# Optimization experiments

Measured on AMD Instinct MI355X. Metric: run time of the kernel, lower is better.

The kernel has to match this reference:

```python
import jax, jax.numpy as jnp
import numpy as np

N, C, H, W = 4, 256, 60, 60
CIMG = 5  # rgb/ir channels after add_position (3 + x + y)
K = 8
ITERS = 2


def setup_inputs() -> dict:
    key = jax.random.key(0)
    ks = jax.random.split(key, 12)
    inp = {
        "cnn_encoder_output": jax.random.normal(ks[0], (N, C, H, W), jnp.float32),
        "rgb": jax.random.normal(ks[1], (N, CIMG, H, W), jnp.float32),
        "ir": jax.random.normal(ks[2], (N, CIMG, H, W), jnp.float32),
        # g-MLP (mlp_num_layers=1): Linear(2C -> C), torch weight layout [out, in]
        "W_g_rgb": jax.random.normal(ks[3], (C, 2 * C), jnp.float32) * 0.02,
        "b_g_rgb": jnp.zeros((C,), jnp.float32),
        "W_g_ir": jax.random.normal(ks[4], (C, 2 * C), jnp.float32) * 0.02,
        "b_g_ir": jnp.zeros((C,), jnp.float32),
        # SE block: Linear(2C -> C//16) -> ReLU -> Linear(C//16 -> C) -> Sigmoid
        "W_se1": jax.random.normal(ks[5], (C // 16, 2 * C), jnp.float32) * 0.02,
        "b_se1": jnp.zeros((C // 16,), jnp.float32),
        "W_se2": jax.random.normal(ks[6], (C, C // 16), jnp.float32) * 0.02,
        "b_se2": jnp.zeros((C,), jnp.float32),
        "gamma": jnp.ones((1,), jnp.float32),
        "gnn_iterations": ITERS,
        "k": K,
    }
    return inp


def _knn_indices(x, k):
    # x: [N, HW, D] -> indices of k nearest neighbours [N, HW, k]
    r = jnp.einsum("nid,njd->nij", x, x)          # gram matrix
    sq = jnp.einsum("nid,nid->ni", x, x)          # squared norms
    d2 = sq[:, :, None] + sq[:, None, :] - 2.0 * r
    d = jnp.sqrt(jnp.maximum(d2, 0.0))
    d = jax.lax.stop_gradient(d)
    _, idx = jax.lax.top_k(-d, k)                  # smallest distances
    return idx


def _gather(h, idx):
    # h: [N, HW, C], idx: [N, HW, K] -> [N, HW, K, C]
    return jax.vmap(lambda hn, i: hn[i])(h, idx)


def reference(cnn_encoder_output, rgb, ir, W_g_rgb, b_g_rgb, W_g_ir, b_g_ir,
              W_se1, b_se1, W_se2, b_se2, gamma, gnn_iterations, k):
    n, c, hh, ww = cnn_encoder_output.shape
    hw = hh * ww
    rgb_f = rgb.reshape(n, rgb.shape[1], hw).transpose(0, 2, 1)  # [N, HW, 5]
    ir_f = ir.reshape(n, ir.shape[1], hw).transpose(0, 2, 1)
    knn_rgb = _knn_indices(rgb_f, k)  # [N, HW, K]
    knn_ir = _knn_indices(ir_f, k)

    h = cnn_encoder_output.transpose(0, 2, 3, 1).reshape(n, hw, c)  # [N, HW, C]

    for _ in range(gnn_iterations):
        rgb_nb = _gather(h, knn_rgb)  # [N, HW, K, C]
        ir_nb = _gather(h, knn_ir)
        rgb_feat = jnp.concatenate([rgb_nb, rgb_nb - ir_nb], axis=-1)  # [N,HW,K,2C]
        ir_feat = jnp.concatenate([ir_nb, ir_nb - rgb_nb], axis=-1)
        m_rgb = jnp.max(jax.nn.relu(jnp.einsum("nhkf,cf->nhkc", rgb_feat, W_g_rgb) + b_g_rgb), axis=2)
        m_ir = jnp.max(jax.nn.relu(jnp.einsum("nhkf,cf->nhkc", ir_feat, W_g_ir) + b_g_ir), axis=2)
        cc = jnp.concatenate([m_rgb, m_ir], axis=-1).mean(axis=1, keepdims=True)  # [N,1,2C]
        se = jax.nn.sigmoid(jax.nn.relu(cc @ W_se1.T + b_se1) @ W_se2.T + b_se2)  # [N,1,C]
        h = se * h

    h = h.reshape(n, hh, ww, c).transpose(0, 3, 1, 2)
    return jax.nn.relu(gamma * h + cnn_encoder_output)
```

## Files before the change

### kernel.cpp

```cpp
#include <hip/hip_runtime.h>
#include <hip/hip_bf16.h>

#define NB 4
#define CH 256
#define HWT 3600
#define KNN 8
#define POSB 16
#define MPAD 3712

#define SSEGP 16
#define CAND 225
#define RB 8

#define GEMM_BLKS 928

typedef __attribute__((ext_vector_type(8))) __bf16 bf16x8;
typedef __attribute__((ext_vector_type(4))) float f32x4;
typedef __attribute__((ext_vector_type(4))) unsigned u32x4;

__device__ inline float med3f(float a, float b, float c) {
    return __builtin_amdgcn_fmed3f(a, b, c);
}

__device__ __forceinline__ void insert8(float* best, float kf) {
    best[7] = med3f(best[6], best[7], kf);
    best[6] = med3f(best[5], best[6], kf);
    best[5] = med3f(best[4], best[5], kf);
    best[4] = med3f(best[3], best[4], kf);
    best[3] = med3f(best[2], best[3], kf);
    best[2] = med3f(best[1], best[2], kf);
    best[1] = med3f(best[0], best[1], kf);
    best[0] = fminf(best[0], kf);
}


__device__ __forceinline__ void gemm_body(int lid, int n,
                                          const __hip_bfloat16* __restrict__ Abf,
                                          const __hip_bfloat16* __restrict__ Wbf,
                                          __hip_bfloat16* __restrict__ Yall,
                                          char* smem) {
    char* sA = smem;
    char* sB = smem + 16384;
    int w = (lid & 7) * 29 + (lid >> 3);
    int m0 = (w >> 3) * 128;
    int o0 = (w & 7) * 128;
    int t = threadIdx.x;
    int lane = t & 63, wid = t >> 6;
    int wm = wid >> 1, wo = wid & 1;

    const __hip_bfloat16* Ab = Abf + (size_t)n * MPAD * CH;
    const __hip_bfloat16* Wb = Wbf + (size_t)n * 1024 * CH;

    f32x4 acc[4][4] = {};

    int srow = t >> 3;
    int sslot = t & 7;
    int swz = (sslot ^ (srow & 7)) << 4;
    int fr = lane & 15;
    int kg = lane >> 4;
    int p = lane & 7;

    uint4 av[4], bv[4];
    auto load_tile = [&](int ks) {
#pragma unroll
        for (int r = 0; r < 4; ++r) {
            int row = srow + 32 * r;
            av[r] = *(const uint4*)(Ab + ((size_t)(m0 + row)) * CH + ks * 64 + sslot * 8);
            bv[r] = *(const uint4*)(Wb + ((size_t)(o0 + row)) * CH + ks * 64 + sslot * 8);
        }
    };
    load_tile(0);

    for (int ks = 0; ks < 4; ++ks) {
        __syncthreads();
#pragma unroll
        for (int r = 0; r < 4; ++r) {
            int row = srow + 32 * r;
            *(uint4*)(sA + row * 128 + swz) = av[r];
            *(uint4*)(sB + row * 128 + swz) = bv[r];
        }
        __syncthreads();
        if (ks < 3) load_tile(ks + 1);
#pragma unroll
        for (int kk = 0; kk < 2; ++kk) {
            bf16x8 hf[4], wf[4];
            int slot = kk * 4 + kg;
            int inrow = (slot ^ p) << 4;
#pragma unroll
            for (int f = 0; f < 4; ++f) {
                hf[f] = *(const bf16x8*)(sA + (wm * 64 + f * 16 + fr) * 128 + inrow);
                wf[f] = *(const bf16x8*)(sB + (wo * 64 + f * 16 + fr) * 128 + inrow);
            }
#pragma unroll
            for (int fa = 0; fa < 4; ++fa)
#pragma unroll
                for (int fb = 0; fb < 4; ++fb)
                    acc[fa][fb] = __builtin_amdgcn_mfma_f32_16x16x32_bf16(
                        wf[fa], hf[fb], acc[fa][fb], 0, 0, 0);
        }
    }

    __syncthreads();
#pragma unroll
    for (int fa = 0; fa < 4; ++fa)
#pragma unroll
        for (int fb = 0; fb < 4; ++fb) {
            int ml = wm * 64 + fb * 16 + fr;
            int ob = (wo * 64 + fa * 16 + kg * 4) * 2;
            f32x4 v = acc[fa][fb];
            union { ushort4 u; __hip_bfloat16 h[4]; } pk;
            pk.h[0] = __float2bfloat16(v.x);
            pk.h[1] = __float2bfloat16(v.y);
            pk.h[2] = __float2bfloat16(v.z);
            pk.h[3] = __float2bfloat16(v.w);
            int swzb = (ob & ~15) ^ ((ml & 15) << 4);
            *(ushort4*)(smem + ml * 256 + swzb + (ob & 15)) = pk.u;
        }
    __syncthreads();
    __hip_bfloat16* Y = Yall + (size_t)n * HWT * 1024;
    int colb = (t & 15) * 16;
#pragma unroll
    for (int i = 0; i < 8; ++i) {
        int row = i * 16 + (t >> 4);
        int grow = m0 + row;
        if (grow < HWT) {
            u32x4 v = *(const u32x4*)(smem + row * 256 + (colb ^ ((row & 15) << 4)));
            __builtin_nontemporal_store(v, (u32x4*)((char*)Y + (size_t)grow * 2048 + o0 * 2 + colb));
        }
    }
}

__global__ __launch_bounds__(256) void gemm_k(const __hip_bfloat16* __restrict__ Abf,
                                              const __hip_bfloat16* __restrict__ Wbf,
                                              __hip_bfloat16* __restrict__ Yall) {
    __shared__ char smem[32768];
    int gid = blockIdx.x;
    gemm_body(gid % 232, gid / 232, Abf, Wbf, Yall, smem);
}

__global__ __launch_bounds__(256) void knn_main(const float* __restrict__ xpack,
                                                unsigned* __restrict__ partial) {
    int seg = blockIdx.x, rb = blockIdx.y, nm = blockIdx.z;
    int t = threadIdx.x;
    const float* xp = xpack + (size_t)nm * HWT * 8;
    __shared__ float4 xs4[CAND];
    __shared__ float2 xs2[CAND];
    int j0 = seg * CAND;
    if (t < CAND) {
        float4 a = ((const float4*)xp)[(size_t)(j0 + t) * 2];
        float4 b = ((const float4*)xp)[(size_t)(j0 + t) * 2 + 1];
        xs4[t] = a;
        xs2[t] = float2{b.x, b.y + 1.0f};
    }
    __syncthreads();

    bool active = (t < CAND);
    int r0 = rb * 450 + t;
    int rr0 = active ? r0 : 0;
    int rr1 = active ? (r0 + CAND) : 0;
    float4 a0 = ((const float4*)xp)[(size_t)rr0 * 2];
    float4 b0 = ((const float4*)xp)[(size_t)rr0 * 2 + 1];
    float4 a1 = ((const float4*)xp)[(size_t)rr1 * 2];
    float4 b1 = ((const float4*)xp)[(size_t)rr1 * 2 + 1];
    float q0 = b0.y, q1 = b1.y;

    const float BIG = __uint_as_float(0x7F000000u);
    float bst0[8], bst1[8];
#pragma unroll
    for (int i = 0; i < 8; ++i) { bst0[i] = BIG; bst1[i] = BIG; }

    unsigned jg0 = (unsigned)j0;
#pragma unroll 5
    for (int jj = 0; jj < CAND; ++jj) {
        float4 a = xs4[jj];
        float2 b = xs2[jj];
        unsigned jg = jg0 + jj;
        float d0 = a.x * a0.x;
        d0 = fmaf(a.y, a0.y, d0);
        d0 = fmaf(a.z, a0.z, d0);
        d0 = fmaf(a.w, a0.w, d0);
        d0 = fmaf(b.x, b0.x, d0);
        float e0 = fmaf(-2.0f, d0, b.y + q0);
        float d1 = a.x * a1.x;
        d1 = fmaf(a.y, a1.y, d1);
        d1 = fmaf(a.z, a1.z, d1);
        d1 = fmaf(a.w, a1.w, d1);
        d1 = fmaf(b.x, b1.x, d1);
        float e1 = fmaf(-2.0f, d1, b.y + q1);
        float k0 = __uint_as_float((__float_as_uint(e0) & 0xFFFFF000u) | jg);
        float k1 = __uint_as_float((__float_as_uint(e1) & 0xFFFFF000u) | jg);
        insert8(bst0, k0);
        insert8(bst1, k1);
    }
    if (active) {
        unsigned* o = partial + (((size_t)(nm * SSEGP + seg)) * HWT + r0) * 8;
        ((uint4*)o)[0] = uint4{ __float_as_uint(bst0[0]), __float_as_uint(bst0[1]),
                                __float_as_uint(bst0[2]), __float_as_uint(bst0[3]) };
        ((uint4*)o)[1] = uint4{ __float_as_uint(bst0[4]), __float_as_uint(bst0[5]),
                                __float_as_uint(bst0[6]), __float_as_uint(bst0[7]) };
        unsigned* o1 = partial + (((size_t)(nm * SSEGP + seg)) * HWT + r0 + CAND) * 8;
        ((uint4*)o1)[0] = uint4{ __float_as_uint(bst1[0]), __float_as_uint(bst1[1]),
                                 __float_as_uint(bst1[2]), __float_as_uint(bst1[3]) };
        ((uint4*)o1)[1] = uint4{ __float_as_uint(bst1[4]), __float_as_uint(bst1[5]),
                                 __float_as_uint(bst1[6]), __float_as_uint(bst1[7]) };
    }
}

__global__ __launch_bounds__(256) void fusedA(const float* __restrict__ cnn,
                                              __hip_bfloat16* __restrict__ Abf,
                                              const float* __restrict__ Wg_rgb,
                                              const float* __restrict__ Wg_ir,
                                              float* __restrict__ Wcomb,
                                              float* __restrict__ g,
                                              __hip_bfloat16* __restrict__ Wbf,
                                              const float* __restrict__ rgb,
                                              const float* __restrict__ ir,
                                              float* __restrict__ xpack) {
    int bid = blockIdx.x;
    int t = threadIdx.x;
    if (bid < GEMM_BLKS) {
        __shared__ float st[64][65];
        int n = bid / 232;
        int rem = bid - n * 232;
        int k0 = (rem / 58) * 64;
        int m0 = (rem % 58) * 64;
        const float* src = cnn + (size_t)n * CH * HWT;
#pragma unroll
        for (int r = 0; r < 4; ++r) {
            int kl = r * 16 + (t >> 4);
            int ms = (t & 15) * 4;
            float4 v = {0.f, 0.f, 0.f, 0.f};
            if (m0 + ms < HWT) v = *(const float4*)(src + (size_t)(k0 + kl) * HWT + m0 + ms);
            st[ms + 0][kl] = v.x; st[ms + 1][kl] = v.y;
            st[ms + 2][kl] = v.z; st[ms + 3][kl] = v.w;
        }
        __syncthreads();
        int m = t >> 2, kg = (t & 3) * 16;
        union { uint4 u[2]; __hip_bfloat16 h[16]; } pk;
#pragma unroll
        for (int i = 0; i < 16; ++i) pk.h[i] = __float2bfloat16(st[m][kg + i]);
        __hip_bfloat16* dst = Abf + ((size_t)n * MPAD + m0 + m) * CH + k0 + kg;
        ((uint4*)dst)[0] = pk.u[0];
        ((uint4*)dst)[1] = pk.u[1];
    } else if (bid < GEMM_BLKS + 1024) {
        int e = (bid - GEMM_BLKS) * 256 + t;
        int o = e >> 8, j = e & 255;
        float v;
        if (o < 256)      v = Wg_rgb[o * 512 + j] + Wg_rgb[o * 512 + 256 + j];
        else if (o < 512) v = Wg_rgb[(o - 256) * 512 + 256 + j];
        else if (o < 768) v = Wg_ir[(o - 512) * 512 + j] + Wg_ir[(o - 512) * 512 + 256 + j];
        else              v = Wg_ir[(o - 768) * 512 + 256 + j];
        Wcomb[e] = v;
        __hip_bfloat16 h = __float2bfloat16(v);
#pragma unroll
        for (int n = 0; n < NB; ++n) Wbf[(size_t)n * 262144 + e] = h;
        if (e < NB * CH) g[e] = 1.0f;
    } else {
        int e = (bid - GEMM_BLKS - 1024) * 256 + t;
        if (e < 2 * NB * HWT) {
            int nm = e / HWT, j = e - nm * HWT;
            int mod = nm / NB, n = nm - mod * NB;
            const float* x = (mod == 0 ? rgb : ir) + (size_t)n * 5 * HWT;
            float v[5], q = 0.f;
#pragma unroll
            for (int d = 0; d < 5; ++d) { v[d] = x[d * HWT + j]; q = fmaf(v[d], v[d], q); }
            float* o = xpack + (size_t)e * 8;
#pragma unroll
            for (int d = 0; d < 5; ++d) o[d] = v[d];
            o[5] = q; o[6] = 0.f; o[7] = 0.f;
        }
    }
}

__global__ __launch_bounds__(256) void knn_merge_zero(const unsigned* __restrict__ partial,
                                                      int* __restrict__ knn_rgb,
                                                      int* __restrict__ knn_ir,
                                                      float* __restrict__ ccsum) {
    int bid = blockIdx.x;
    if (bid >= 450) {
        int e = (bid - 450) * 256 + threadIdx.x;
        if (e < NB * 512) ccsum[e] = 0.f;
        return;
    }
    int tid = bid * 256 + threadIdx.x;
    int rid = tid >> 1, sub = tid & 1;
    int nm = rid / HWT, row = rid - nm * HWT;
    const float BIG = __uint_as_float(0x7F000000u);
    float best[8];
#pragma unroll
    for (int i = 0; i < 8; ++i) best[i] = BIG;
    for (int s = sub; s < SSEGP; s += 2) {
        const unsigned* p = partial + (((size_t)(nm * SSEGP + s)) * HWT + row) * 8;
#pragma unroll
        for (int w = 0; w < 2; ++w) {
            uint4 v = ((const uint4*)p)[w];
            unsigned vv[4] = { v.x, v.y, v.z, v.w };
#pragma unroll
            for (int e = 0; e < 4; ++e) insert8(best, __uint_as_float(vv[e]));
        }
    }
    float other[8];
#pragma unroll
    for (int i = 0; i < 8; ++i) other[i] = __shfl_xor(best[i], 1);
#pragma unroll
    for (int i = 0; i < 8; ++i) insert8(best, other[i]);
    if (sub == 0) {
        int mod = nm / NB, n = nm - mod * NB;
        int* o = (mod == 0 ? knn_rgb : knn_ir) + ((size_t)n * HWT + row) * KNN;
#pragma unroll
        for (int i = 0; i < 8; ++i) o[i] = (int)(__float_as_uint(best[i]) & 0xFFFu);
    }
}

__global__ __launch_bounds__(256) void scale_w_zero(const float* __restrict__ Wcomb,
                                                    const float* __restrict__ g,
                                                    __hip_bfloat16* __restrict__ Wbf,
                                                    float* __restrict__ ccsum) {
    int bid = blockIdx.x;
    if (bid >= 512) {
        int e = (bid - 512) * 256 + threadIdx.x;
        if (e < NB * 512) ccsum[e] = 0.f;
        return;
    }
    int n = bid >> 7;
    int gid = (bid & 127) * 256 + threadIdx.x;
    int o = gid >> 5;
    int kb = (gid & 31) * 8;
    const float* w = Wcomb + o * 256 + kb;
    const float* gp = g + n * CH + kb;
    union { uint4 u; __hip_bfloat16 h[8]; } pk;
#pragma unroll
    for (int i = 0; i < 8; ++i) pk.h[i] = __float2bfloat16(w[i] * gp[i]);
    *(uint4*)(Wbf + ((size_t)n * 1024 + o) * CH + kb) = pk.u;
}

__global__ __launch_bounds__(256) void gather_kernel(const __hip_bfloat16* __restrict__ Yall,
                                                     const int* __restrict__ knn_rgb,
                                                     const int* __restrict__ knn_ir,
                                                     const float* __restrict__ b_rgb,
                                                     const float* __restrict__ b_ir,
                                                     float* __restrict__ ccsum) {
    int lid = blockIdx.x;
    int xcd = lid & 7, sub = lid >> 3;
    int wg = (xcd < 4 ? xcd * 113 : 4 * 113 + (xcd - 4) * 112) + sub;
    int n = wg / 225;
    int hwbase = (wg - n * 225) * POSB;
    int t = threadIdx.x;
    int half = t >> 7;
    int cp = (t & 127) << 1;
    __shared__ int sidx[POSB][2][KNN];
    {
        int p = t >> 4, rem = t & 15;
        int hw = hwbase + p;
        int v;
        if (rem < 8) v = knn_rgb[((size_t)n * HWT + hw) * KNN + rem];
        else         v = knn_ir[((size_t)n * HWT + hw) * KNN + (rem - 8)];
        sidx[p][rem >> 3][rem & 7] = v;
    }
    __syncthreads();
    const float* bias = half ? b_ir : b_rgb;
    float b0 = bias[cp], b1 = bias[cp + 1];
    float acc0 = 0.f, acc1 = 0.f;
    const __hip_bfloat16* Y = Yall + (size_t)n * HWT * 1024;
    int offA = half * 512 + cp;
    int offB = half * 512 + 256 + cp;
    for (int p = 0; p < POSB; ++p) {
        float m0 = 0.f, m1 = 0.f;
#pragma unroll
        for (int k = 0; k < KNN; ++k) {
            int jA = sidx[p][half][k];
            int jB = sidx[p][half ^ 1][k];
            unsigned u1 = *(const unsigned*)(Y + (size_t)jA * 1024 + offA);
            unsigned u2 = *(const unsigned*)(Y + (size_t)jB * 1024 + offB);
            float a0 = __uint_as_float(u1 << 16);
            float a1 = __uint_as_float(u1 & 0xFFFF0000u);
            float c0 = __uint_as_float(u2 << 16);
            float c1 = __uint_as_float(u2 & 0xFFFF0000u);
            m0 = fmaxf(m0, a0 - c0 + b0);
            m1 = fmaxf(m1, a1 - c1 + b1);
        }
        acc0 += m0;
        acc1 += m1;
    }
    atomicAdd(&ccsum[n * 512 + half * 256 + cp], acc0);
    atomicAdd(&ccsum[n * 512 + half * 256 + cp + 1], acc1);
}

__global__ __launch_bounds__(256) void se_kernel(const float* __restrict__ ccsum,
                                                 const float* __restrict__ W1,
                                                 const float* __restrict__ b1,
                                                 const float* __restrict__ W2,
                                                 const float* __restrict__ b2,
                                                 float* __restrict__ g) {
    int n = blockIdx.x;
    int t = threadIdx.x;
    __shared__ float hid[16];
    __shared__ float cc[512];
    cc[t] = ccsum[n * 512 + t] * (1.0f / HWT);
    cc[256 + t] = ccsum[n * 512 + 256 + t] * (1.0f / HWT);
    __syncthreads();
    if (t < 16) {
        float s = b1[t];
        for (int j = 0; j < 512; ++j) s = fmaf(W1[t * 512 + j], cc[j], s);
        hid[t] = fmaxf(s, 0.f);
    }
    __syncthreads();
    float s = b2[t];
#pragma unroll
    for (int q = 0; q < 16; ++q) s = fmaf(W2[t * 16 + q], hid[q], s);
    float se = 1.0f / (1.0f + expf(-s));
    g[n * CH + t] *= se;
}

__global__ void final_kernel(const float* __restrict__ cnn, const float* __restrict__ g,
                             const float* __restrict__ gamma, float* __restrict__ out) {
    int t = blockIdx.x * blockDim.x + threadIdx.x;
    if (t >= NB * CH * HWT / 4) return;
    int nc = (t * 4) / HWT;
    float4 x = ((const float4*)cnn)[t];
    float s = gamma[0] * g[nc] + 1.0f;
    float4 o;
    o.x = fmaxf(s * x.x, 0.f);
    o.y = fmaxf(s * x.y, 0.f);
    o.z = fmaxf(s * x.z, 0.f);
    o.w = fmaxf(s * x.w, 0.f);
    ((float4*)out)[t] = o;
}

extern "C" void kernel_launch(void* const* d_in, const int* in_sizes, int n_in,
                              void* d_out, int out_size, void* d_ws, size_t ws_size,
                              hipStream_t stream) {
    const float* cnn    = (const float*)d_in[0];
    const float* rgb    = (const float*)d_in[1];
    const float* ir     = (const float*)d_in[2];
    const float* Wg_rgb = (const float*)d_in[3];
    const float* bg_rgb = (const float*)d_in[4];
    const float* Wg_ir  = (const float*)d_in[5];
    const float* bg_ir  = (const float*)d_in[6];
    const float* Wse1   = (const float*)d_in[7];
    const float* bse1   = (const float*)d_in[8];
    const float* Wse2   = (const float*)d_in[9];
    const float* bse2   = (const float*)d_in[10];
    const float* gamma  = (const float*)d_in[11];
    float* out = (float*)d_out;

    char* ws = (char*)d_ws;
    size_t off = 0;
    float* xpack = (float*)(ws + off); off += (size_t)2 * NB * HWT * 8 * 4;
    int* knn_rgb = (int*)(ws + off); off += (size_t)NB * HWT * KNN * 4;
    int* knn_ir  = (int*)(ws + off); off += (size_t)NB * HWT * KNN * 4;
    float* Wcomb = (float*)(ws + off); off += (size_t)1024 * 256 * 4;
    __hip_bfloat16* Wbf = (__hip_bfloat16*)(ws + off); off += (size_t)NB * 1024 * CH * 2;
    __hip_bfloat16* Abf = (__hip_bfloat16*)(ws + off); off += (size_t)NB * MPAD * CH * 2;
    __hip_bfloat16* Yall = (__hip_bfloat16*)(ws + off); off += (size_t)NB * HWT * 1024 * 2;
    unsigned* partial = (unsigned*)(ws + off);
    off += (size_t)2 * NB * SSEGP * HWT * 8 * 4;
    float* ccsum = (float*)(ws + off); off += (size_t)NB * 512 * 4;
    float* g     = (float*)(ws + off); off += (size_t)NB * CH * 4;

    fusedA<<<GEMM_BLKS + 1024 + 113, 256, 0, stream>>>(cnn, Abf, Wg_rgb, Wg_ir, Wcomb, g,
                                                       Wbf, rgb, ir, xpack);
    knn_main<<<dim3(SSEGP, RB, 2 * NB), 256, 0, stream>>>(xpack, partial);
    gemm_k<<<GEMM_BLKS, 256, 0, stream>>>(Abf, Wbf, Yall);
    knn_merge_zero<<<458, 256, 0, stream>>>(partial, knn_rgb, knn_ir, ccsum);
    gather_kernel<<<900, 256, 0, stream>>>(Yall, knn_rgb, knn_ir, bg_rgb, bg_ir, ccsum);
    se_kernel<<<NB, 256, 0, stream>>>(ccsum, Wse1, bse1, Wse2, bse2, g);
    scale_w_zero<<<520, 256, 0, stream>>>(Wcomb, g, Wbf, ccsum);
    gemm_k<<<GEMM_BLKS, 256, 0, stream>>>(Abf, Wbf, Yall);
    gather_kernel<<<900, 256, 0, stream>>>(Yall, knn_rgb, knn_ir, bg_rgb, bg_ir, ccsum);
    se_kernel<<<NB, 256, 0, stream>>>(ccsum, Wse1, bse1, Wse2, bse2, g);
    final_kernel<<<3600, 256, 0, stream>>>(cnn, g, gamma, out);
}
```

Before: 226.4 us.

## Split gather over channel halves and position halves; vectorize kNN distance math

The gather kernel now runs as two launches, each covering half the channels. Inside each block, two thread groups each handle 8 of the 16 positions, and their partial sums are combined through shared memory before the atomic add. The aim is more parallelism and more in-flight loads per position in this latency-bound random gather. The cost is double the launches and double the index loads. Separately, the kNN distance loop now computes its two rows with float2 vector arithmetic, so the compiler can emit packed FP32 operations.

Result: slower. 257.1 us (+13.6%).

```diff
diff --git a/kernel.cpp b/kernel.cpp
--- a/kernel.cpp
+++ b/kernel.cpp
@@ -5,7 +5,6 @@
 #define CH 256
 #define HWT 3600
 #define KNN 8
-#define POSB 16
 #define MPAD 3712
 
 #define SSEGP 16
@@ -16,6 +15,8 @@
 
 typedef __attribute__((ext_vector_type(8))) __bf16 bf16x8;
 typedef __attribute__((ext_vector_type(4))) float f32x4;
+typedef __attribute__((ext_vector_type(2))) float f32x2;
+typedef __attribute__((ext_vector_type(2))) unsigned u32x2;
 typedef __attribute__((ext_vector_type(4))) unsigned u32x4;
 
 __device__ inline float med3f(float a, float b, float c) {
@@ -162,7 +163,12 @@
     float4 b0 = ((const float4*)xp)[(size_t)rr0 * 2 + 1];
     float4 a1 = ((const float4*)xp)[(size_t)rr1 * 2];
     float4 b1 = ((const float4*)xp)[(size_t)rr1 * 2 + 1];
-    float q0 = b0.y, q1 = b1.y;
+    f32x2 rx = {a0.x, a1.x};
+    f32x2 ry = {a0.y, a1.y};
+    f32x2 rz = {a0.z, a1.z};
+    f32x2 rw = {a0.w, a1.w};
+    f32x2 rv = {b0.x, b1.x};
+    f32x2 rq = {b0.y, b1.y};
 
     const float BIG = __uint_as_float(0x7F000000u);
     float bst0[8], bst1[8];
@@ -175,20 +181,16 @@
         float4 a = xs4[jj];
         float2 b = xs2[jj];
         unsigned jg = jg0 + jj;
-        float d0 = a.x * a0.x;
-        d0 = fmaf(a.y, a0.y, d0);
-        d0 = fmaf(a.z, a0.z, d0);
-        d0 = fmaf(a.w, a0.w, d0);
-        d0 = fmaf(b.x, b0.x, d0);
-        float e0 = fmaf(-2.0f, d0, b.y + q0);
-        float d1 = a.x * a1.x;
-        d1 = fmaf(a.y, a1.y, d1);
-        d1 = fmaf(a.z, a1.z, d1);
-        d1 = fmaf(a.w, a1.w, d1);
-        d1 = fmaf(b.x, b1.x, d1);
-        float e1 = fmaf(-2.0f, d1, b.y + q1);
-        float k0 = __uint_as_float((__float_as_uint(e0) & 0xFFFFF000u) | jg);
-        float k1 = __uint_as_float((__float_as_uint(e1) & 0xFFFFF000u) | jg);
+        f32x2 d = rx * a.x;
+        d += ry * a.y;
+        d += rz * a.z;
+        d += rw * a.w;
+        d += rv * b.x;
+        f32x2 e = (rq + b.y) - 2.0f * d;
+        u32x2 u;
+        __builtin_memcpy(&u, &e, 8);
+        float k0 = __uint_as_float((u.x & 0xFFFFF000u) | jg);
+        float k1 = __uint_as_float((u.y & 0xFFFFF000u) | jg);
         insert8(bst0, k0);
         insert8(bst1, k1);
     }
@@ -339,16 +341,19 @@
                                                      const int* __restrict__ knn_ir,
                                                      const float* __restrict__ b_rgb,
                                                      const float* __restrict__ b_ir,
-                                                     float* __restrict__ ccsum) {
+                                                     float* __restrict__ ccsum, int hc) {
     int lid = blockIdx.x;
-    int xcd = lid & 7, sub = lid >> 3;
-    int wg = (xcd < 4 ? xcd * 113 : 4 * 113 + (xcd - 4) * 112) + sub;
+    int xcd = lid & 7, sub_ = lid >> 3;
+    int wg = (xcd < 4 ? xcd * 113 : 452 + (xcd - 4) * 112) + sub_;
     int n = wg / 225;
-    int hwbase = (wg - n * 225) * POSB;
+    int hwbase = (wg - n * 225) * 16;
     int t = threadIdx.x;
     int half = t >> 7;
-    int cp = (t & 127) << 1;
-    __shared__ int sidx[POSB][2][KNN];
+    int psub = (t >> 6) & 1;
+    int pr = t & 63;
+    int cp = hc * 128 + pr * 2;
+    __shared__ int sidx[16][2][KNN];
+    __shared__ float red[2][64][2];
     {
         int p = t >> 4, rem = t & 15;
         int hw = hwbase + p;
@@ -359,12 +364,12 @@
     }
     __syncthreads();
     const float* bias = half ? b_ir : b_rgb;
-    float b0 = bias[cp], b1 = bias[cp + 1];
+    float bb0 = bias[cp], bb1 = bias[cp + 1];
     float acc0 = 0.f, acc1 = 0.f;
     const __hip_bfloat16* Y = Yall + (size_t)n * HWT * 1024;
     int offA = half * 512 + cp;
     int offB = half * 512 + 256 + cp;
-    for (int p = 0; p < POSB; ++p) {
+    for (int p = psub * 8; p < psub * 8 + 8; ++p) {
         float m0 = 0.f, m1 = 0.f;
 #pragma unroll
         for (int k = 0; k < KNN; ++k) {
@@ -376,14 +381,20 @@
             float a1 = __uint_as_float(u1 & 0xFFFF0000u);
             float c0 = __uint_as_float(u2 << 16);
             float c1 = __uint_as_float(u2 & 0xFFFF0000u);
-            m0 = fmaxf(m0, a0 - c0 + b0);
-            m1 = fmaxf(m1, a1 - c1 + b1);
+            m0 = fmaxf(m0, a0 - c0 + bb0);
+            m1 = fmaxf(m1, a1 - c1 + bb1);
         }
         acc0 += m0;
         acc1 += m1;
     }
-    atomicAdd(&ccsum[n * 512 + half * 256 + cp], acc0);
-    atomicAdd(&ccsum[n * 512 + half * 256 + cp + 1], acc1);
+    if (psub) { red[half][pr][0] = acc0; red[half][pr][1] = acc1; }
+    __syncthreads();
+    if (!psub) {
+        acc0 += red[half][pr][0];
+        acc1 += red[half][pr][1];
+        atomicAdd(&ccsum[n * 512 + half * 256 + cp], acc0);
+        atomicAdd(&ccsum[n * 512 + half * 256 + cp + 1], acc1);
+    }
 }
 
 __global__ __launch_bounds__(256) void se_kernel(const float* __restrict__ ccsum,
@@ -463,11 +474,13 @@
     knn_main<<<dim3(SSEGP, RB, 2 * NB), 256, 0, stream>>>(xpack, partial);
     gemm_k<<<GEMM_BLKS, 256, 0, stream>>>(Abf, Wbf, Yall);
     knn_merge_zero<<<458, 256, 0, stream>>>(partial, knn_rgb, knn_ir, ccsum);
-    gather_kernel<<<900, 256, 0, stream>>>(Yall, knn_rgb, knn_ir, bg_rgb, bg_ir, ccsum);
+    gather_kernel<<<900, 256, 0, stream>>>(Yall, knn_rgb, knn_ir, bg_rgb, bg_ir, ccsum, 0);
+    gather_kernel<<<900, 256, 0, stream>>>(Yall, knn_rgb, knn_ir, bg_rgb, bg_ir, ccsum, 1);
     se_kernel<<<NB, 256, 0, stream>>>(ccsum, Wse1, bse1, Wse2, bse2, g);
     scale_w_zero<<<520, 256, 0, stream>>>(Wcomb, g, Wbf, ccsum);
     gemm_k<<<GEMM_BLKS, 256, 0, stream>>>(Abf, Wbf, Yall);
-    gather_kernel<<<900, 256, 0, stream>>>(Yall, knn_rgb, knn_ir, bg_rgb, bg_ir, ccsum);
+    gather_kernel<<<900, 256, 0, stream>>>(Yall, knn_rgb, knn_ir, bg_rgb, bg_ir, ccsum, 0);
+    gather_kernel<<<900, 256, 0, stream>>>(Yall, knn_rgb, knn_ir, bg_rgb, bg_ir, ccsum, 1);
     se_kernel<<<NB, 256, 0, stream>>>(ccsum, Wse1, bse1, Wse2, bse2, g);
     final_kernel<<<3600, 256, 0, stream>>>(cnn, g, gamma, out);
 }
```
